# Performance work log

Hardware: AMD Instinct MI355X
Metric: run time of the kernel (lower is better)

The kernel has to match this reference:

```python
import jax, jax.numpy as jnp
import numpy as np


def _inside_quad(pts9, quads):
    """Ray-casting point-in-polygon test (semantics of the pointsJf CUDA kernel),
    evaluated only for matched (diagonal) point/box pairs.

    pts9:  [N, 9, 2] points
    quads: [N, 8] polygon corners (x1,y1,x2,y2,x3,y3,x4,y4)
    returns inside flag [N, 9] float32 in {0.0, 1.0}
    """
    vx = quads[:, 0::2][:, None, :]          # [N,1,4]
    vy = quads[:, 1::2][:, None, :]          # [N,1,4]
    vxj = jnp.roll(vx, 1, axis=-1)           # previous vertex (j = i-1 mod 4)
    vyj = jnp.roll(vy, 1, axis=-1)
    px = pts9[..., 0:1]                      # [N,9,1]
    py = pts9[..., 1:2]                      # [N,9,1]
    straddles = (vy > py) != (vyj > py)      # edge crosses horizontal ray
    # x coordinate of edge at height py (only meaningful where straddles)
    x_int = (vxj - vx) * (py - vy) / (vyj - vy) + vx
    crossings = straddles & (px < x_int)     # [N,9,4] bool
    inside = (jnp.sum(crossings.astype(jnp.int32), axis=-1) % 2)
    return inside.astype(jnp.float32)        # [N,9]


def _spatial_border_loss(pts, gt_bboxes, weight, loss_weight):
    n = pts.shape[0]
    pts9 = pts.reshape(n, 9, 2)
    inside = _inside_quad(pts9, gt_bboxes)                    # [N,9]
    out_mask = (inside == 0.0).astype(pts.dtype)              # points outside their gt box
    cx = (gt_bboxes[:, 0] + gt_bboxes[:, 4]) * 0.5
    cy = (gt_bboxes[:, 1] + gt_bboxes[:, 5]) * 0.5
    center = jnp.stack([cx, cy], axis=1)[:, None, :]          # [N,1,2]
    dist = 0.2 * jnp.sqrt(jnp.sum((pts9 - center) ** 2, axis=-1))  # [N,9]
    cnt = jnp.sum(out_mask)
    loss_sb = jnp.where(cnt > 0, jnp.sum(dist * out_mask) / jnp.maximum(cnt, 1.0), 0.0)
    # weighted_spatial_border_loss: avg_factor = sum(weight_repeated4 > 0)/4 + 1e-6
    avg_factor = jnp.sum((weight > 0).astype(jnp.float32)) + 1e-6
    return loss_weight * (loss_sb / avg_factor)[None]          # shape [1]


def setup_inputs() -> dict:
    key = jax.random.key(0)
    k1, k2, k3 = jax.random.split(key, 3)
    N = 1_000_000
    pts = jax.random.normal(k1, (N, 18), dtype=jnp.float32)
    gt_bboxes = jax.random.normal(k2, (N, 8), dtype=jnp.float32)
    weight = jax.random.uniform(k3, (N,), dtype=jnp.float32)
    return {"pts": pts, "gt_bboxes": gt_bboxes, "weight": weight}


def reference(pts, gt_bboxes, weight):
    return _spatial_border_loss(pts, gt_bboxes, weight, loss_weight=1.0)
```

## Files before the change

kernel.cpp:

```cpp
#include <hip/hip_runtime.h>
#include <cstdint>


#define SBL_BLOCK 512
#define SBL_TILE  512
#define SBL_WAVES (SBL_BLOCK / 64)
#define SBL_WAVE_BYTES (64 * 72)

__global__ void __launch_bounds__(SBL_BLOCK) sbl_main(
    const float* __restrict__ pts,
    const float* __restrict__ quads,
    const float* __restrict__ weight,
    double* __restrict__ part_sum,
    unsigned int* __restrict__ part_cnt,
    unsigned int* __restrict__ part_wpos,
    int n)
{
    __shared__ __align__(16) float s_pts[SBL_TILE * 18];

    const int tid  = threadIdx.x;
    const int lane = tid & 63;
    const int wave = tid >> 6;
    const int base = blockIdx.x * SBL_TILE;
    int rows = n - base; if (rows > SBL_TILE) rows = SBL_TILE;
    const bool have_row = (tid < rows);
    const bool full = (rows == SBL_TILE);

    if (full) {
        const char* g0 = (const char*)pts + (size_t)base * 72
                       + (size_t)wave * SBL_WAVE_BYTES;
        const uint32_t l0 = (uint32_t)(uintptr_t)(void*)s_pts
                          + (uint32_t)(wave * SBL_WAVE_BYTES);
        #pragma unroll
        for (int i = 0; i < 4; ++i) {
            __builtin_amdgcn_global_load_lds(
                (const __attribute__((address_space(1))) void*)(g0 + i * 1024 + lane * 16),
                (__attribute__((address_space(3))) void*)(uintptr_t)(l0 + i * 1024 + lane * 16),
                16, 0, 0);
        }
        #pragma unroll
        for (int j = 0; j < 2; ++j) {
            __builtin_amdgcn_global_load_lds(
                (const __attribute__((address_space(1))) void*)(g0 + 4096 + j * 256 + lane * 4),
                (__attribute__((address_space(3))) void*)(uintptr_t)(l0 + 4096 + j * 256 + lane * 4),
                4, 0, 0);
        }
    } else {
        const float2* g2 = reinterpret_cast<const float2*>(pts + (size_t)base * 18);
        float2* s2 = reinterpret_cast<float2*>(s_pts);
        const int nf2 = rows * 9;
        for (int idx = tid; idx < nf2; idx += SBL_BLOCK) s2[idx] = g2[idx];
    }

    float4 qa = make_float4(0.f, 0.f, 0.f, 0.f);
    float4 qb = make_float4(0.f, 0.f, 0.f, 0.f);
    float wv = 0.0f;
    if (have_row) {
        const float4* q4 = reinterpret_cast<const float4*>(quads) + (size_t)(base + tid) * 2;
        qa = q4[0];
        qb = q4[1];
        wv = weight[base + tid];
    }

    if (full) {
        asm volatile("s_waitcnt vmcnt(0) lgkmcnt(0)" ::: "memory");
        __builtin_amdgcn_sched_barrier(0);
    } else {
        __syncthreads();
    }

    float local_sum = 0.0f;
    unsigned int pack = (wv > 0.0f) ? (1u << 16) : 0u;

    if (have_row) {
        const float vx0 = qa.x, vy0 = qa.y, vx1 = qa.z, vy1 = qa.w;
        const float vx2 = qb.x, vy2 = qb.y, vx3 = qb.z, vy3 = qb.w;
        const float cx = (vx0 + vx2) * 0.5f;
        const float cy = (vy0 + vy2) * 0.5f;
        const float d0 = vy3 - vy0, d1 = vy0 - vy1, d2 = vy1 - vy2, d3 = vy2 - vy3;
        const float e0 = vx3 - vx0, e1 = vx0 - vx1, e2 = vx1 - vx2, e3 = vx2 - vx3;
        const bool  n0 = d0 < 0.0f, n1 = d1 < 0.0f, n2 = d2 < 0.0f, n3 = d3 < 0.0f;

        const float2* prow = reinterpret_cast<const float2*>(s_pts + tid * 18);
        #pragma unroll
        for (int k = 0; k < 9; ++k) {
            const float2 p = prow[k];
            const float px = p.x, py = p.y;

            const bool c0 = vy0 > py, c1 = vy1 > py, c2 = vy2 > py, c3 = vy3 > py;
            const bool s0 = c0 != c3, s1 = c1 != c0, s2 = c2 != c1, s3 = c3 != c2;

            const float t0 = py - vy0, t1 = py - vy1, t2 = py - vy2, t3 = py - vy3;
            const float m0 = e0 * t0, m1 = e1 * t1, m2 = e2 * t2, m3 = e3 * t3;
            const float l0 = (px - vx0) * d0, l1 = (px - vx1) * d1;
            const float l2 = (px - vx2) * d2, l3 = (px - vx3) * d3;

            const bool x0 = s0 && ((l0 < m0) != n0);
            const bool x1 = s1 && ((l1 < m1) != n1);
            const bool x2 = s2 && ((l2 < m2) != n2);
            const bool x3 = s3 && ((l3 < m3) != n3);

            const bool inside = (x0 != x1) != (x2 != x3);
            if (!inside) {
                const float dx = px - cx;
                const float dy = py - cy;
                local_sum += sqrtf(fmaf(dx, dx, dy * dy));
                pack += 1u;
            }
        }
    }

    #pragma unroll
    for (int off = 32; off > 0; off >>= 1) {
        local_sum += __shfl_down(local_sum, off, 64);
        pack      += __shfl_down(pack, off, 64);
    }

    __shared__ float        r_sum[SBL_WAVES];
    __shared__ unsigned int r_pack[SBL_WAVES];
    if (lane == 0) { r_sum[wave] = local_sum; r_pack[wave] = pack; }
    __syncthreads();
    if (tid == 0) {
        double bsum = 0.0;
        unsigned int bcnt = 0u, bwpos = 0u;
        #pragma unroll
        for (int i = 0; i < SBL_WAVES; ++i) {
            bsum  += (double)r_sum[i];
            bcnt  += r_pack[i] & 0xffffu;
            bwpos += r_pack[i] >> 16;
        }
        part_sum[blockIdx.x]  = bsum;
        part_cnt[blockIdx.x]  = bcnt;
        part_wpos[blockIdx.x] = bwpos;
    }
}

__global__ void __launch_bounds__(1024) sbl_finalize(
    const double* __restrict__ part_sum,
    const unsigned int* __restrict__ part_cnt,
    const unsigned int* __restrict__ part_wpos,
    float* __restrict__ out,
    int nblocks)
{
    const int tid = threadIdx.x;
    double s = 0.0;
    unsigned int c = 0u, w = 0u;
    for (int i = tid; i < nblocks; i += 1024) {
        s += part_sum[i];
        c += part_cnt[i];
        w += part_wpos[i];
    }
    #pragma unroll
    for (int off = 32; off > 0; off >>= 1) {
        s += __shfl_down(s, off, 64);
        c += __shfl_down(c, off, 64);
        w += __shfl_down(w, off, 64);
    }
    __shared__ double       fs[16];
    __shared__ unsigned int fc[16], fw[16];
    const int lane = tid & 63, wave = tid >> 6;
    if (lane == 0) { fs[wave] = s; fc[wave] = c; fw[wave] = w; }
    __syncthreads();
    if (tid == 0) {
        double ts = 0.0; unsigned int tc = 0u, tw = 0u;
        #pragma unroll
        for (int k = 0; k < 16; ++k) { ts += fs[k]; tc += fc[k]; tw += fw[k]; }
        const double loss_sb = (tc > 0u) ? (0.2 * ts / (double)tc) : 0.0;
        const double avg_factor = (double)tw + 1e-6;
        out[0] = (float)(loss_sb / avg_factor);
    }
}

extern "C" void kernel_launch(void* const* d_in, const int* in_sizes, int n_in,
                              void* d_out, int out_size, void* d_ws, size_t ws_size,
                              hipStream_t stream) {
    const float* pts    = (const float*)d_in[0];
    const float* quads  = (const float*)d_in[1];
    const float* weight = (const float*)d_in[2];
    float* out = (float*)d_out;

    const int n = in_sizes[2];
    const int nblocks = (n + SBL_TILE - 1) / SBL_TILE;

    double*       part_sum  = (double*)d_ws;
    unsigned int* part_cnt  = (unsigned int*)((char*)d_ws + (size_t)nblocks * sizeof(double));
    unsigned int* part_wpos = (unsigned int*)((char*)d_ws + (size_t)nblocks * (sizeof(double) + sizeof(unsigned int)));

    sbl_main<<<nblocks, SBL_BLOCK, 0, stream>>>(pts, quads, weight,
                                                part_sum, part_cnt, part_wpos, n);
    sbl_finalize<<<1, 1024, 0, stream>>>(part_sum, part_cnt, part_wpos, out, nblocks);
}
```

Before: 133.3 us.

## Use persistent grid with double-buffered LDS prefetch of point tiles

Replaces the one-tile-per-block launch with a fixed grid of 1024 blocks of 256 threads that loop over tiles. Each block prefetches the next tile's points into a second LDS buffer with direct global-to-LDS loads, plus the next quads and weights into registers, while computing the current tile. The aim is to overlap memory latency with compute and to shrink the finalize reduction to a fixed number of partials. In exchange, LDS use per block doubles and correctness depends on a hand-counted vmcnt wait value. With a fixed grid, wave-level parallelism is bounded by the grid size.

```diff
diff --git a/kernel.cpp b/kernel.cpp
--- a/kernel.cpp
+++ b/kernel.cpp
@@ -2,10 +2,72 @@
 #include <cstdint>
 
 
-#define SBL_BLOCK 512
-#define SBL_TILE  512
+#define SBL_BLOCK 256
+#define SBL_TILE  256
+#define SBL_GRID  1024
 #define SBL_WAVES (SBL_BLOCK / 64)
 #define SBL_WAVE_BYTES (64 * 72)
+#define SBL_BUF_FLOATS (SBL_TILE * 18)
+
+__device__ __forceinline__ void sbl_issue_dma(const float* pts, int tile_base,
+                                              int wave, int lane, uint32_t lds_byte)
+{
+    const char* g0 = (const char*)pts + (size_t)tile_base * 72 + (size_t)wave * SBL_WAVE_BYTES;
+    const uint32_t l0 = lds_byte + (uint32_t)(wave * SBL_WAVE_BYTES);
+    #pragma unroll
+    for (int i = 0; i < 4; ++i) {
+        __builtin_amdgcn_global_load_lds(
+            (const __attribute__((address_space(1))) void*)(g0 + i * 1024 + lane * 16),
+            (__attribute__((address_space(3))) void*)(uintptr_t)(l0 + i * 1024 + lane * 16),
+            16, 0, 0);
+    }
+    #pragma unroll
+    for (int j = 0; j < 2; ++j) {
+        __builtin_amdgcn_global_load_lds(
+            (const __attribute__((address_space(1))) void*)(g0 + 4096 + j * 256 + lane * 4),
+            (__attribute__((address_space(3))) void*)(uintptr_t)(l0 + 4096 + j * 256 + lane * 4),
+            4, 0, 0);
+    }
+}
+
+__device__ __forceinline__ void sbl_compute_row(const float2* prow, float4 qa, float4 qb,
+                                                float& local_sum, unsigned int& pack)
+{
+    const float vx0 = qa.x, vy0 = qa.y, vx1 = qa.z, vy1 = qa.w;
+    const float vx2 = qb.x, vy2 = qb.y, vx3 = qb.z, vy3 = qb.w;
+    const float cx = (vx0 + vx2) * 0.5f;
+    const float cy = (vy0 + vy2) * 0.5f;
+    const float d0 = vy3 - vy0, d1 = vy0 - vy1, d2 = vy1 - vy2, d3 = vy2 - vy3;
+    const float e0 = vx3 - vx0, e1 = vx0 - vx1, e2 = vx1 - vx2, e3 = vx2 - vx3;
+    const bool  n0 = d0 < 0.0f, n1 = d1 < 0.0f, n2 = d2 < 0.0f, n3 = d3 < 0.0f;
+
+    #pragma unroll
+    for (int k = 0; k < 9; ++k) {
+        const float2 p = prow[k];
+        const float px = p.x, py = p.y;
+
+        const bool c0 = vy0 > py, c1 = vy1 > py, c2 = vy2 > py, c3 = vy3 > py;
+        const bool s0 = c0 != c3, s1 = c1 != c0, s2 = c2 != c1, s3 = c3 != c2;
+
+        const float t0 = py - vy0, t1 = py - vy1, t2 = py - vy2, t3 = py - vy3;
+        const float m0 = e0 * t0, m1 = e1 * t1, m2 = e2 * t2, m3 = e3 * t3;
+        const float l0 = (px - vx0) * d0, l1 = (px - vx1) * d1;
+        const float l2 = (px - vx2) * d2, l3 = (px - vx3) * d3;
+
+        const bool x0 = s0 && ((l0 < m0) != n0);
+        const bool x1 = s1 && ((l1 < m1) != n1);
+        const bool x2 = s2 && ((l2 < m2) != n2);
+        const bool x3 = s3 && ((l3 < m3) != n3);
+
+        const bool inside = (x0 != x1) != (x2 != x3);
+        if (!inside) {
+            const float dx = px - cx;
+            const float dy = py - cy;
+            local_sum += sqrtf(fmaf(dx, dx, dy * dy));
+            pack += 1u;
+        }
+    }
+}
 
 __global__ void __launch_bounds__(SBL_BLOCK) sbl_main(
     const float* __restrict__ pts,
@@ -16,97 +78,79 @@
     unsigned int* __restrict__ part_wpos,
     int n)
 {
-    __shared__ __align__(16) float s_pts[SBL_TILE * 18];
+    __shared__ __align__(16) float s_pts[2 * SBL_BUF_FLOATS];
 
     const int tid  = threadIdx.x;
     const int lane = tid & 63;
     const int wave = tid >> 6;
-    const int base = blockIdx.x * SBL_TILE;
-    int rows = n - base; if (rows > SBL_TILE) rows = SBL_TILE;
-    const bool have_row = (tid < rows);
-    const bool full = (rows == SBL_TILE);
-
-    if (full) {
-        const char* g0 = (const char*)pts + (size_t)base * 72
-                       + (size_t)wave * SBL_WAVE_BYTES;
-        const uint32_t l0 = (uint32_t)(uintptr_t)(void*)s_pts
-                          + (uint32_t)(wave * SBL_WAVE_BYTES);
-        #pragma unroll
-        for (int i = 0; i < 4; ++i) {
-            __builtin_amdgcn_global_load_lds(
-                (const __attribute__((address_space(1))) void*)(g0 + i * 1024 + lane * 16),
-                (__attribute__((address_space(3))) void*)(uintptr_t)(l0 + i * 1024 + lane * 16),
-                16, 0, 0);
-        }
-        #pragma unroll
-        for (int j = 0; j < 2; ++j) {
-            __builtin_amdgcn_global_load_lds(
-                (const __attribute__((address_space(1))) void*)(g0 + 4096 + j * 256 + lane * 4),
-                (__attribute__((address_space(3))) void*)(uintptr_t)(l0 + 4096 + j * 256 + lane * 4),
-                4, 0, 0);
-        }
-    } else {
+    const int bid  = blockIdx.x;
+    const int ntiles_full = n / SBL_TILE;
+
+    float local_sum = 0.0f;
+    unsigned int pack = 0u;
+    const uint32_t lds0 = (uint32_t)(uintptr_t)(void*)s_pts;
+
+    int t = bid;
+    if (t < ntiles_full) {
+        sbl_issue_dma(pts, t * SBL_TILE, wave, lane, lds0);
+        {
+            const int r = t * SBL_TILE + tid;
+            const float4* q4 = reinterpret_cast<const float4*>(quads) + (size_t)r * 2;
+            float4 qa_c = q4[0];
+            float4 qb_c = q4[1];
+            float  wv_c = weight[r];
+            int parity = 0;
+
+            while (true) {
+                const int  tn = t + SBL_GRID;
+                const bool has_next = (tn < ntiles_full);
+                float4 qa_n = make_float4(0.f, 0.f, 0.f, 0.f);
+                float4 qb_n = make_float4(0.f, 0.f, 0.f, 0.f);
+                float  wv_n = 0.0f;
+                if (has_next) {
+                    sbl_issue_dma(pts, tn * SBL_TILE, wave, lane,
+                                  lds0 + (uint32_t)((parity ^ 1) * (SBL_BUF_FLOATS * 4)));
+                    const int rn = tn * SBL_TILE + tid;
+                    const float4* q4n = reinterpret_cast<const float4*>(quads) + (size_t)rn * 2;
+                    qa_n = q4n[0];
+                    qb_n = q4n[1];
+                    wv_n = weight[rn];
+                    asm volatile("s_waitcnt vmcnt(9)" ::: "memory");
+                } else {
+                    asm volatile("s_waitcnt vmcnt(0)" ::: "memory");
+                }
+                __builtin_amdgcn_sched_barrier(0);
+
+                pack += (wv_c > 0.0f) ? (1u << 16) : 0u;
+                const float2* prow = reinterpret_cast<const float2*>(
+                    s_pts + parity * SBL_BUF_FLOATS + tid * 18);
+                sbl_compute_row(prow, qa_c, qb_c, local_sum, pack);
+
+                if (!has_next) break;
+                t = tn; parity ^= 1;
+                qa_c = qa_n; qb_c = qb_n; wv_c = wv_n;
+            }
+        }
+    }
+
+    const int ttail = ntiles_full;
+    if ((size_t)ttail * SBL_TILE < (size_t)n && (ttail % SBL_GRID) == bid) {
+        const int base = ttail * SBL_TILE;
+        const int rows = n - base;
+        __syncthreads();
         const float2* g2 = reinterpret_cast<const float2*>(pts + (size_t)base * 18);
         float2* s2 = reinterpret_cast<float2*>(s_pts);
-        const int nf2 = rows * 9;
-        for (int idx = tid; idx < nf2; idx += SBL_BLOCK) s2[idx] = g2[idx];
-    }
-
-    float4 qa = make_float4(0.f, 0.f, 0.f, 0.f);
-    float4 qb = make_float4(0.f, 0.f, 0.f, 0.f);
-    float wv = 0.0f;
-    if (have_row) {
-        const float4* q4 = reinterpret_cast<const float4*>(quads) + (size_t)(base + tid) * 2;
-        qa = q4[0];
-        qb = q4[1];
-        wv = weight[base + tid];
-    }
-
-    if (full) {
-        asm volatile("s_waitcnt vmcnt(0) lgkmcnt(0)" ::: "memory");
-        __builtin_amdgcn_sched_barrier(0);
-    } else {
+        for (int idx = tid; idx < rows * 9; idx += SBL_BLOCK) s2[idx] = g2[idx];
         __syncthreads();
-    }
-
-    float local_sum = 0.0f;
-    unsigned int pack = (wv > 0.0f) ? (1u << 16) : 0u;
-
-    if (have_row) {
-        const float vx0 = qa.x, vy0 = qa.y, vx1 = qa.z, vy1 = qa.w;
-        const float vx2 = qb.x, vy2 = qb.y, vx3 = qb.z, vy3 = qb.w;
-        const float cx = (vx0 + vx2) * 0.5f;
-        const float cy = (vy0 + vy2) * 0.5f;
-        const float d0 = vy3 - vy0, d1 = vy0 - vy1, d2 = vy1 - vy2, d3 = vy2 - vy3;
-        const float e0 = vx3 - vx0, e1 = vx0 - vx1, e2 = vx1 - vx2, e3 = vx2 - vx3;
-        const bool  n0 = d0 < 0.0f, n1 = d1 < 0.0f, n2 = d2 < 0.0f, n3 = d3 < 0.0f;
-
-        const float2* prow = reinterpret_cast<const float2*>(s_pts + tid * 18);
-        #pragma unroll
-        for (int k = 0; k < 9; ++k) {
-            const float2 p = prow[k];
-            const float px = p.x, py = p.y;
-
-            const bool c0 = vy0 > py, c1 = vy1 > py, c2 = vy2 > py, c3 = vy3 > py;
-            const bool s0 = c0 != c3, s1 = c1 != c0, s2 = c2 != c1, s3 = c3 != c2;
-
-            const float t0 = py - vy0, t1 = py - vy1, t2 = py - vy2, t3 = py - vy3;
-            const float m0 = e0 * t0, m1 = e1 * t1, m2 = e2 * t2, m3 = e3 * t3;
-            const float l0 = (px - vx0) * d0, l1 = (px - vx1) * d1;
-            const float l2 = (px - vx2) * d2, l3 = (px - vx3) * d3;
-
-            const bool x0 = s0 && ((l0 < m0) != n0);
-            const bool x1 = s1 && ((l1 < m1) != n1);
-            const bool x2 = s2 && ((l2 < m2) != n2);
-            const bool x3 = s3 && ((l3 < m3) != n3);
-
-            const bool inside = (x0 != x1) != (x2 != x3);
-            if (!inside) {
-                const float dx = px - cx;
-                const float dy = py - cy;
-                local_sum += sqrtf(fmaf(dx, dx, dy * dy));
-                pack += 1u;
-            }
+        if (tid < rows) {
+            const int r = base + tid;
+            const float4* q4 = reinterpret_cast<const float4*>(quads) + (size_t)r * 2;
+            const float4 qa = q4[0];
+            const float4 qb = q4[1];
+            const float  wv = weight[r];
+            pack += (wv > 0.0f) ? (1u << 16) : 0u;
+            const float2* prow = reinterpret_cast<const float2*>(s_pts + tid * 18);
+            sbl_compute_row(prow, qa, qb, local_sum, pack);
         }
     }
 
@@ -129,9 +173,9 @@
             bcnt  += r_pack[i] & 0xffffu;
             bwpos += r_pack[i] >> 16;
         }
-        part_sum[blockIdx.x]  = bsum;
-        part_cnt[blockIdx.x]  = bcnt;
-        part_wpos[blockIdx.x] = bwpos;
+        part_sum[bid]  = bsum;
+        part_cnt[bid]  = bcnt;
+        part_wpos[bid] = bwpos;
     }
 }
 
@@ -180,13 +224,12 @@
     float* out = (float*)d_out;
 
     const int n = in_sizes[2];
-    const int nblocks = (n + SBL_TILE - 1) / SBL_TILE;
 
     double*       part_sum  = (double*)d_ws;
-    unsigned int* part_cnt  = (unsigned int*)((char*)d_ws + (size_t)nblocks * sizeof(double));
-    unsigned int* part_wpos = (unsigned int*)((char*)d_ws + (size_t)nblocks * (sizeof(double) + sizeof(unsigned int)));
-
-    sbl_main<<<nblocks, SBL_BLOCK, 0, stream>>>(pts, quads, weight,
-                                                part_sum, part_cnt, part_wpos, n);
-    sbl_finalize<<<1, 1024, 0, stream>>>(part_sum, part_cnt, part_wpos, out, nblocks);
-}
+    unsigned int* part_cnt  = (unsigned int*)((char*)d_ws + (size_t)SBL_GRID * sizeof(double));
+    unsigned int* part_wpos = (unsigned int*)((char*)d_ws + (size_t)SBL_GRID * (sizeof(double) + sizeof(unsigned int)));
+
+    sbl_main<<<SBL_GRID, SBL_BLOCK, 0, stream>>>(pts, quads, weight,
+                                                 part_sum, part_cnt, part_wpos, n);
+    sbl_finalize<<<1, 1024, 0, stream>>>(part_sum, part_cnt, part_wpos, out, SBL_GRID);
+}
```

Result: slower. 138.8 us (+4.2%).
